# Kernel tuning notes

Hardware: AMD Instinct MI355X
Metric: run time of the kernel (lower is better)

Reference implementation:

```python
import jax, jax.numpy as jnp
import numpy as np

LRELU_SLOPE = 0.2
SQRT2 = 1.4142135623730951

def make_coord(h, w):
    # LIIF make_coord: cell-center coords in [-1, 1]; index 0 is the row (dim -2) coord.
    ys = -1.0 + (2.0 * jnp.arange(h, dtype=jnp.float32) + 1.0) / h
    xs = -1.0 + (2.0 * jnp.arange(w, dtype=jnp.float32) + 1.0) / w
    yy, xx = jnp.meshgrid(ys, xs, indexing='ij')
    return jnp.stack([yy, xx], axis=-1).reshape(h * w, 2)  # [Q, 2]

def style_layer(x, style_vec, scale2, shift, mod_w, mod_b, conv_w, act_b):
    # StyleGAN2-style modulated 3x3 conv + instance norm + (scale2, shift) affine + fused leaky relu.
    s = style_vec @ mod_w.T + mod_b                                   # [B, Cin] modulation
    w = conv_w[None] * s[:, None, :, None, None]                      # [B, Cout, Cin, 3, 3]
    demod = jax.lax.rsqrt(jnp.sum(w * w, axis=(2, 3, 4)) + 1e-8)      # [B, Cout]
    y = jax.lax.conv_general_dilated(x * s[:, :, None, None], conv_w, (1, 1), 'SAME',
                                     dimension_numbers=('NCHW', 'OIHW', 'NCHW'))
    y = y * demod[:, :, None, None]
    mu = jnp.mean(y, axis=(2, 3), keepdims=True)
    var = jnp.var(y, axis=(2, 3), keepdims=True)
    y = (y - mu) * jax.lax.rsqrt(var + 1e-5)                          # InstanceNorm2d (no affine)
    y = y * scale2 + shift
    return jax.nn.leaky_relu(y + act_b[None, :, None, None], LRELU_SLOPE) * SQRT2

def reference(x, scale1, scale2, shift, mod_w, mod_b, conv_w, act_b, w1, b1, w2, b2, out_h, out_w):
    B, C, Hf, Wf = x.shape
    feat = style_layer(x, scale1, scale2, shift, mod_w, mod_b, conv_w, act_b)
    Q = out_h * out_w
    coord = jnp.broadcast_to(make_coord(out_h, out_w)[None], (B, Q, 2))  # [B, Q, 2]
    rx = 1.0 / Hf  # = 2/Hf/2
    ry = 1.0 / Wf
    eps_shift = 1e-6
    feat_flat = feat.reshape(B, C, Hf * Wf).transpose(0, 2, 1)  # [B, Hf*Wf, C]
    preds, areas = [], []
    for vx in (-1, 1):
        for vy in (-1, 1):
            cy = jnp.clip(coord[..., 0] + vx * rx + eps_shift, -1.0 + 1e-6, 1.0 - 1e-6)
            cx = jnp.clip(coord[..., 1] + vy * ry + eps_shift, -1.0 + 1e-6, 1.0 - 1e-6)
            # nearest grid_sample (align_corners=False): idx = floor((c+1)/2 * size)
            iy = jnp.clip(jnp.floor((cy + 1.0) * 0.5 * Hf), 0, Hf - 1).astype(jnp.int32)
            ix = jnp.clip(jnp.floor((cx + 1.0) * 0.5 * Wf), 0, Wf - 1).astype(jnp.int32)
            lin = iy * Wf + ix                                        # [B, Q]
            q_feat = jnp.take_along_axis(feat_flat, lin[..., None], axis=1)  # [B, Q, C]
            qy = -1.0 + (2.0 * iy.astype(jnp.float32) + 1.0) / Hf     # nearest feat-cell coord
            qx = -1.0 + (2.0 * ix.astype(jnp.float32) + 1.0) / Wf
            rel_y = (coord[..., 0] - qy) * Hf
            rel_x = (coord[..., 1] - qx) * Wf
            inp = jnp.concatenate([q_feat, rel_y[..., None], rel_x[..., None]], axis=-1)  # [B,Q,C+2]
            pred = (inp @ w1 + b1) @ w2 + b2                          # two stacked Linears, no act
            preds.append(pred)
            areas.append(jnp.abs(rel_y * rel_x) + 1e-9)
    tot_area = areas[0] + areas[1] + areas[2] + areas[3]
    areas = [areas[3], areas[2], areas[1], areas[0]]  # diagonal swap (local ensemble)
    ret = jnp.zeros_like(preds[0])
    for pred, area in zip(preds, areas):
        ret = ret + pred * (area / tot_area)[..., None]
    return ret  # [B, Q, dim]

def setup_inputs() -> dict:
    key = jax.random.key(0)
    ks = jax.random.split(key, 12)
    B, C, Hf, Wf, S = 4, 64, 64, 64, 512
    return {
        'x': jax.random.normal(ks[0], (B, C, Hf, Wf), jnp.float32),
        'scale1': jax.random.normal(ks[1], (B, S), jnp.float32),
        'scale2': jax.random.normal(ks[2], (B, C, 1, 1), jnp.float32),
        'shift': jax.random.normal(ks[3], (B, C, 1, 1), jnp.float32),
        'mod_w': jax.random.normal(ks[4], (C, S), jnp.float32) * 0.02,
        'mod_b': jnp.ones((C,), jnp.float32),
        'conv_w': jax.random.normal(ks[5], (C, C, 3, 3), jnp.float32) * 0.05,
        'act_b': jax.random.normal(ks[6], (C,), jnp.float32) * 0.02,
        'w1': jax.random.normal(ks[7], (C + 2, 256), jnp.float32) * 0.05,
        'b1': jax.random.normal(ks[8], (256,), jnp.float32) * 0.01,
        'w2': jax.random.normal(ks[9], (256, C), jnp.float32) * 0.05,
        'b2': jax.random.normal(ks[10], (C,), jnp.float32) * 0.01,
        'out_h': 256,
        'out_w': 256,
    }
```

## Files before the change

### kernel.cpp

```cpp
#include <hip/hip_runtime.h>

#define SQRT2F 1.41421356237309515f

typedef __attribute__((ext_vector_type(8))) short bf16x8;
typedef __attribute__((ext_vector_type(4))) float f32x4;

enum : int {
  DM_OFF   = 0,
  BC_OFF   = 256,
  WC_OFF   = 1024,
  P_OFF    = 8192,
  Y_OFF    = 65536,
  WS_FLOATS = Y_OFF + 1048576
};

__device__ __align__(16) float WS[WS_FLOATS];
__device__ __align__(256) unsigned bar_cnt[64];
__device__ __align__(256) unsigned bar_gen[64];

__device__ __forceinline__ unsigned ld_llcu(const unsigned* p) {
  unsigned v;
  asm volatile("global_load_dword %0, %1, off sc0 sc1\n\ts_waitcnt vmcnt(0)"
               : "=v"(v) : "v"(p) : "memory");
  return v;
}
__device__ __forceinline__ float ld_llcf(const float* p) {
  float v;
  asm volatile("global_load_dword %0, %1, off sc0 sc1\n\ts_waitcnt vmcnt(0)"
               : "=v"(v) : "v"(p) : "memory");
  return v;
}
__device__ __forceinline__ void ld_llc4_nw(const float* p, f32x4& v) {
  asm volatile("global_load_dwordx4 %0, %1, off sc0 sc1"
               : "=v"(v) : "v"(p) : "memory");
}
__device__ __forceinline__ void llc_wait() {
  asm volatile("s_waitcnt vmcnt(0)" ::: "memory");
}
__device__ __forceinline__ void stg_llc1(float* p, float v) {
  asm volatile("global_store_dword %0, %1, off sc0 sc1"
               :: "v"(p), "v"(v) : "memory");
}
__device__ __forceinline__ void stg_llc4(float* p, f32x4 v) {
  asm volatile("global_store_dwordx4 %0, %1, off sc0 sc1"
               :: "v"(p), "v"(v) : "memory");
}

struct ConvSh {
  unsigned short Xl[3 * 66 * 64];
  unsigned short Wl[64 * 24 * 8];
  float part[512];
  float s_sh[64];
};
struct GoutSh {
  unsigned short ftb[128][72];
  unsigned short WcTb[64][72];
  float G[100][68];
  float red[2048];
  float A[64], B[64], bcl[64];
};
union ShU { ConvSh c; GoutSh g; };

__device__ __forceinline__ unsigned short f2bf(float v) {
  unsigned int u = __float_as_uint(v);
  u += 0x7fffu + ((u >> 16) & 1u);
  return (unsigned short)(u >> 16);
}

__global__ __launch_bounds__(512) void mega_kernel(
    const float* __restrict__ x,      const float* __restrict__ scale1,
    const float* __restrict__ scale2, const float* __restrict__ shiftp,
    const float* __restrict__ mod_w,  const float* __restrict__ mod_b,
    const float* __restrict__ conv_w, const float* __restrict__ act_b,
    const float* __restrict__ b1,     const float* __restrict__ w2,
    const float* __restrict__ b2,     const float* __restrict__ w1,
    float* __restrict__ out) {
  const int bid = blockIdx.x;
  const int b = bid >> 6;
  const int r = bid & 63;
  const int t = threadIdx.x;
  const int w = t >> 6, lane = t & 63;
  const int l15 = lane & 15, l4 = lane >> 4;

  __shared__ __align__(16) ShU sh;

  {
    const int i = t >> 3, qq = t & 7;
    const float* sv = scale1 + b * 512 + qq * 64;
    const float* mw = mod_w + i * 512 + qq * 64;
    float p = 0.f;
    for (int k = 0; k < 64; ++k) p = fmaf(sv[k], mw[k], p);
    sh.c.part[t] = p;
  }
  __syncthreads();
  if ((t & 7) == 0) {
    const int i = t >> 3;
    float s = mod_b[i];
    #pragma unroll
    for (int k = 0; k < 8; ++k) s += sh.c.part[t + k];
    sh.c.s_sh[i] = s;
  }
  __syncthreads();

  if (r == 0) {
    const int o = t >> 3, qq = t & 7;
    const float* cw = conv_w + o * 576 + qq * 72;
    float d = 0.f;
    #pragma unroll
    for (int ii = 0; ii < 8; ++ii) {
      const float ss = sh.c.s_sh[qq * 8 + ii];
      float wsq = 0.f;
      #pragma unroll
      for (int k = 0; k < 9; ++k) { const float wv = cw[ii * 9 + k]; wsq += wv * wv; }
      d += ss * ss * wsq;
    }
    sh.c.part[t] = d;
    __syncthreads();
    if ((t & 7) == 0) {
      float dd = 1e-8f;
      #pragma unroll
      for (int k = 0; k < 8; ++k) dd += sh.c.part[t + k];
      stg_llc1(&WS[DM_OFF + b * 64 + (t >> 3)], rsqrtf(dd));
    }
    __syncthreads();
  }

  {
    int4* Xz = (int4*)sh.c.Xl;
    int4 z; z.x = z.y = z.z = z.w = 0;
    for (int idx = t; idx < 1584; idx += 512) Xz[idx] = z;
  }
  __syncthreads();

  {
    const int col = t & 63;
    const int tq = t >> 6;
    unsigned int* Xw = (unsigned int*)sh.c.Xl;
    #pragma unroll
    for (int it = 0; it < 12; ++it) {
      const int task = it * 8 + tq;
      const int row3 = task >> 5;
      const int ich = (task & 31) * 2;
      const int rr = r - 1 + row3;
      if (rr >= 0 && rr < 64) {
        const float* xb = x + ((size_t)(b * 64 + ich) << 12) + (rr << 6) + col;
        const float v0 = xb[0] * sh.c.s_sh[ich];
        const float v1 = xb[4096] * sh.c.s_sh[ich + 1];
        const unsigned int u = (unsigned int)f2bf(v0) | ((unsigned int)f2bf(v1) << 16);
        const int colp = col + 1;
        const int byte = ((row3 * 66 + colp) << 7) + ((((ich >> 3)) ^ (colp & 7)) << 4) + ((ich & 7) << 1);
        Xw[byte >> 2] = u;
      }
    }
  }

  const int oh = w >> 2, pg = w & 3;
  f32x4 acc[2];
  acc[0] = (f32x4){0.f, 0.f, 0.f, 0.f};
  acc[1] = (f32x4){0.f, 0.f, 0.f, 0.f};

  const bf16x8* Xv = (const bf16x8*)sh.c.Xl;
  const bf16x8* Wv = (const bf16x8*)sh.c.Wl;
  int4* Wst = (int4*)sh.c.Wl;

  for (int dy = 0; dy < 3; ++dy) {
    __syncthreads();
    #pragma unroll
    for (int i = 0; i < 3; ++i) {
      const int idx = i * 512 + t;
      const int o = idx / 24;
      const int g = idx - o * 24;
      const int dx = g >> 3, gg = g & 7;
      const float* cw = conv_w + o * 576 + (gg * 8) * 9 + dy * 3 + dx;
      int4 v;
      v.x = (int)((unsigned int)f2bf(cw[0])  | ((unsigned int)f2bf(cw[9])  << 16));
      v.y = (int)((unsigned int)f2bf(cw[18]) | ((unsigned int)f2bf(cw[27]) << 16));
      v.z = (int)((unsigned int)f2bf(cw[36]) | ((unsigned int)f2bf(cw[45]) << 16));
      v.w = (int)((unsigned int)f2bf(cw[54]) | ((unsigned int)f2bf(cw[63]) << 16));
      Wst[o * 24 + dx * 8 + (gg ^ (o & 7))] = v;
    }
    __syncthreads();

    #pragma unroll
    for (int dx = 0; dx < 3; ++dx) {
      #pragma unroll
      for (int kh = 0; kh < 2; ++kh) {
        const int kg = kh * 4 + l4;
        bf16x8 afr[2];
        #pragma unroll
        for (int m = 0; m < 2; ++m) {
          const int o = oh * 32 + m * 16 + l15;
          afr[m] = Wv[o * 24 + dx * 8 + (kg ^ (o & 7))];
        }
        const int colp = pg * 16 + l15 + dx;
        const bf16x8 bfr = Xv[((dy * 66 + colp) << 3) + (kg ^ (colp & 7))];
        #pragma unroll
        for (int m = 0; m < 2; ++m)
          acc[m] = __builtin_amdgcn_mfma_f32_16x16x32_bf16(
              afr[m], bfr, acc[m], 0, 0, 0);
      }
    }
  }

  {
    const int px = pg * 16 + l15;
    float* yq = WS + Y_OFF + (((size_t)b * 4096 + r * 64 + px) << 6);
    #pragma unroll
    for (int m = 0; m < 2; ++m)
      stg_llc4(yq + oh * 32 + m * 16 + l4 * 4, acc[m]);
  }

  __syncthreads();
  {
    float* sred = sh.c.part;
    #pragma unroll
    for (int m = 0; m < 2; ++m) {
      #pragma unroll
      for (int j = 0; j < 4; ++j) {
        float s1 = acc[m][j];
        float s2 = acc[m][j] * acc[m][j];
        #pragma unroll
        for (int off = 1; off < 16; off <<= 1) {
          s1 += __shfl_xor(s1, off);
          s2 += __shfl_xor(s2, off);
        }
        if (l15 == 0) {
          const int ol = m * 16 + l4 * 4 + j;
          sred[(w * 32 + ol) * 2 + 0] = s1;
          sred[(w * 32 + ol) * 2 + 1] = s2;
        }
      }
    }
    __syncthreads();
    if (t < 128) {
      const int o = t >> 1, wh = t & 1;
      const int ohh = o >> 5, ol = o & 31;
      float s = 0.f;
      #pragma unroll
      for (int pq = 0; pq < 4; ++pq)
        s += sred[(((ohh * 4 + pq) * 32) + ol) * 2 + wh];
      stg_llc1(&WS[P_OFF + (((size_t)b * 64 + r) * 64 + o) * 2 + wh], s);
    }
  }

  if (t < 17) {
    const int idx = t * 256 + bid;
    if (idx < 4224) {
      const int c = idx >> 6, o = idx & 63;
      const float* r1 = w1 + c * 256;
      float a = 0.f;
      for (int k = 0; k < 256; ++k) a = fmaf(r1[k], w2[k * 64 + o], a);
      stg_llc1(&WS[WC_OFF + idx], a);
    } else if (idx < 4288) {
      const int o = idx - 4224;
      float a = 0.f;
      for (int k = 0; k < 256; ++k) a = fmaf(b1[k], w2[k * 64 + o], a);
      stg_llc1(&WS[BC_OFF + o], a + b2[o]);
    }
  }

  asm volatile("s_waitcnt vmcnt(0)" ::: "memory");
  __syncthreads();
  if (t == 0) {
    unsigned* cnt = &bar_cnt[0];
    unsigned* gen = &bar_gen[0];
    const unsigned g0 = ld_llcu(gen);
    const unsigned old = __hip_atomic_fetch_add(cnt, 1u, __ATOMIC_RELAXED,
                                                __HIP_MEMORY_SCOPE_AGENT);
    if (old == 255u) {
      __hip_atomic_store(cnt, 0u, __ATOMIC_RELAXED, __HIP_MEMORY_SCOPE_AGENT);
      __hip_atomic_fetch_add(gen, 1u, __ATOMIC_RELAXED,
                             __HIP_MEMORY_SCOPE_AGENT);
    } else {
      while (ld_llcu(gen) == g0) __builtin_amdgcn_s_sleep(8);
    }
  }
  __syncthreads();

  const int ty = (bid >> 3) & 7;
  const int tx = bid & 7;
  const int cy_base = ty * 8 - 1, cx_base = tx * 8 - 1;
  float* WcL = &sh.g.G[0][0];

  f32x4 pv0, pv1, pv2, pv3, wv0, wv1, wv2, yv[4];
  int ycell[4], ycq[4];
  bool yok[4];
  {
    const float* Pb = WS + P_OFF + (size_t)b * 8192;
    ld_llc4_nw(Pb + (size_t)t * 4, pv0);
    ld_llc4_nw(Pb + (size_t)(t + 512) * 4, pv1);
    ld_llc4_nw(Pb + (size_t)(t + 1024) * 4, pv2);
    ld_llc4_nw(Pb + (size_t)(t + 1536) * 4, pv3);
    ld_llc4_nw(WS + WC_OFF + (size_t)t * 4, wv0);
    ld_llc4_nw(WS + WC_OFF + (size_t)(t + 512) * 4, wv1);
    const int i4 = 1024 + t;
    const float* wp2 = (i4 < 1056) ? (WS + WC_OFF + (size_t)i4 * 4)
                     : (i4 < 1072) ? (WS + BC_OFF + (size_t)(i4 - 1056) * 4)
                                   : (WS + WC_OFF);
    ld_llc4_nw(wp2, wv2);
    const float* yb = WS + Y_OFF + ((size_t)b << 18);
    #pragma unroll
    for (int k = 0; k < 4; ++k) {
      const int f = t + k * 512;
      const int cell = f >> 4, cq = f & 15;
      const int li = cell / 10, lj = cell - li * 10;
      const int ciy = cy_base + li, cix = cx_base + lj;
      const bool ok = (f < 1600) && ciy >= 0 && ciy < 64 && cix >= 0 && cix < 64;
      ycell[k] = cell; ycq[k] = cq; yok[k] = ok;
      const float* ya = ok ? (yb + (((size_t)(ciy << 6) + cix) << 6) + cq * 4) : yb;
      ld_llc4_nw(ya, yv[k]);
    }
    llc_wait();
  }

  {
    const f32x4 ps = pv0 + pv1 + pv2 + pv3;
    *(f32x4*)&sh.g.red[(t >> 5) * 128 + (t & 31) * 4] = ps;
    *(f32x4*)&WcL[t * 4] = wv0;
    *(f32x4*)&WcL[(t + 512) * 4] = wv1;
    if (1024 + t < 1072) *(f32x4*)&WcL[(1024 + t) * 4] = wv2;
  }
  __syncthreads();

  const int sub = t & 3, chb = sub * 16;
  float4 wa[4], wb[4];
  #pragma unroll
  for (int k = 0; k < 4; ++k) {
    wa[k] = *(const float4*)&WcL[64 * 64 + chb + k * 4];
    wb[k] = *(const float4*)&WcL[65 * 64 + chb + k * 4];
  }
  if (t < 64) {
    float S1 = 0.f, S2 = 0.f;
    #pragma unroll
    for (int m = 0; m < 16; ++m) {
      S1 += sh.g.red[m * 128 + t * 2];
      S2 += sh.g.red[m * 128 + t * 2 + 1];
    }
    const float mu = S1 * (1.f / 4096.f);
    const float var = S2 * (1.f / 4096.f) - mu * mu;
    const float dm = ld_llcf(WS + DM_OFF + b * 64 + t);
    const float rstd = rsqrtf(dm * dm * var + 1e-5f);
    const float A = dm * rstd * scale2[b * 64 + t];
    sh.g.A[t] = A;
    sh.g.B[t] = -mu * A + shiftp[b * 64 + t] + act_b[t];
    sh.g.bcl[t] = WcL[4224 + t];
  }
  {
    const int o = t >> 3, g = t & 7;
    int4 pk;
    unsigned int e0, e1, e2, e3;
    e0 = (unsigned int)f2bf(WcL[(g * 8 + 0) * 64 + o]) |
         ((unsigned int)f2bf(WcL[(g * 8 + 1) * 64 + o]) << 16);
    e1 = (unsigned int)f2bf(WcL[(g * 8 + 2) * 64 + o]) |
         ((unsigned int)f2bf(WcL[(g * 8 + 3) * 64 + o]) << 16);
    e2 = (unsigned int)f2bf(WcL[(g * 8 + 4) * 64 + o]) |
         ((unsigned int)f2bf(WcL[(g * 8 + 5) * 64 + o]) << 16);
    e3 = (unsigned int)f2bf(WcL[(g * 8 + 6) * 64 + o]) |
         ((unsigned int)f2bf(WcL[(g * 8 + 7) * 64 + o]) << 16);
    pk.x = (int)e0; pk.y = (int)e1; pk.z = (int)e2; pk.w = (int)e3;
    *(int4*)&sh.g.WcTb[o][g * 8] = pk;
  }
  __syncthreads();

  {
    const float4* A4 = (const float4*)sh.g.A;
    const float4* B4 = (const float4*)sh.g.B;
    #pragma unroll
    for (int k = 0; k < 4; ++k) {
      if (yok[k]) {
        const float4 Av = A4[ycq[k]], Bv = B4[ycq[k]];
        float f0, f1, f2, f3, u;
        u = yv[k][0] * Av.x + Bv.x; f0 = (u > 0.f ? u : 0.2f * u) * SQRT2F;
        u = yv[k][1] * Av.y + Bv.y; f1 = (u > 0.f ? u : 0.2f * u) * SQRT2F;
        u = yv[k][2] * Av.z + Bv.z; f2 = (u > 0.f ? u : 0.2f * u) * SQRT2F;
        u = yv[k][3] * Av.w + Bv.w; f3 = (u > 0.f ? u : 0.2f * u) * SQRT2F;
        uint2 u2;
        u2.x = (unsigned int)f2bf(f0) | ((unsigned int)f2bf(f1) << 16);
        u2.y = (unsigned int)f2bf(f2) | ((unsigned int)f2bf(f3) << 16);
        *(uint2*)&sh.g.ftb[ycell[k]][ycq[k] * 4] = u2;
      }
    }
  }
  __syncthreads();

  if (w < 7) {
    bf16x8 afr[2];
    #pragma unroll
    for (int kt = 0; kt < 2; ++kt)
      afr[kt] = *(const bf16x8*)&sh.g.ftb[w * 16 + l15][kt * 32 + l4 * 8];
    #pragma unroll
    for (int n = 0; n < 4; ++n) {
      const float bcv = sh.g.bcl[n * 16 + l15];
      f32x4 gacc = (f32x4){bcv, bcv, bcv, bcv};
      #pragma unroll
      for (int kt = 0; kt < 2; ++kt) {
        const bf16x8 bfr =
            *(const bf16x8*)&sh.g.WcTb[n * 16 + l15][kt * 32 + l4 * 8];
        gacc = __builtin_amdgcn_mfma_f32_16x16x32_bf16(afr[kt], bfr, gacc, 0, 0, 0);
      }
      #pragma unroll
      for (int j = 0; j < 4; ++j) {
        const int row = w * 16 + l4 * 4 + j;
        if (row < 100) sh.g.G[row][n * 16 + l15] = gacc[j];
      }
    }
  }
  __syncthreads();

  const float lo = -1.f + 1e-6f, hi = 1.f - 1e-6f;
  #pragma unroll 1
  for (int pass = 0; pass < 8; ++pass) {
    const int qi = pass * 128 + (t >> 2);
    const int oy = (ty << 5) + (qi >> 5), ox = (tx << 5) + (qi & 31);

    const float cy0 = -1.f + (2.f * oy + 1.f) * (1.f / 256.f);
    const float cx0 = -1.f + (2.f * ox + 1.f) * (1.f / 256.f);

    int lcell[4];
    float area[4], rely[4], relx[4];
    int j = 0;
    #pragma unroll
    for (int vx = -1; vx <= 1; vx += 2) {
      #pragma unroll
      for (int vy = -1; vy <= 1; vy += 2) {
        float cy = cy0 + (float)vx * (1.f / 64.f) + 1e-6f;
        cy = fminf(fmaxf(cy, lo), hi);
        float cx = cx0 + (float)vy * (1.f / 64.f) + 1e-6f;
        cx = fminf(fmaxf(cx, lo), hi);
        const float fy = floorf((cy + 1.f) * 32.f);
        const float fx = floorf((cx + 1.f) * 32.f);
        const int iy = (int)fminf(fmaxf(fy, 0.f), 63.f);
        const int ix = (int)fminf(fmaxf(fx, 0.f), 63.f);
        const float qy = -1.f + (2.f * iy + 1.f) * (1.f / 64.f);
        const float qx = -1.f + (2.f * ix + 1.f) * (1.f / 64.f);
        const float ry_ = (cy0 - qy) * 64.f;
        const float rx_ = (cx0 - qx) * 64.f;
        lcell[j] = (iy - cy_base) * 10 + (ix - cx_base);
        rely[j] = ry_; relx[j] = rx_;
        area[j] = fabsf(ry_ * rx_) + 1e-9f;
        ++j;
      }
    }
    const float tot = area[0] + area[1] + area[2] + area[3];
    float wgt[4];
    #pragma unroll
    for (int k = 0; k < 4; ++k) wgt[k] = area[3 - k] / tot;
    const float swy = wgt[0] * rely[0] + wgt[1] * rely[1] + wgt[2] * rely[2] + wgt[3] * rely[3];
    const float swx = wgt[0] * relx[0] + wgt[1] * relx[1] + wgt[2] * relx[2] + wgt[3] * relx[3];

    float4 rr[4];
    #pragma unroll
    for (int k = 0; k < 4; ++k) {
      rr[k].x = swy * wa[k].x + swx * wb[k].x;
      rr[k].y = swy * wa[k].y + swx * wb[k].y;
      rr[k].z = swy * wa[k].z + swx * wb[k].z;
      rr[k].w = swy * wa[k].w + swx * wb[k].w;
    }
    #pragma unroll
    for (int jj = 0; jj < 4; ++jj) {
      const float4* gp = (const float4*)&sh.g.G[lcell[jj]][chb];
      const float wv = wgt[jj];
      #pragma unroll
      for (int k = 0; k < 4; ++k) {
        const float4 gv = gp[k];
        rr[k].x += wv * gv.x; rr[k].y += wv * gv.y;
        rr[k].z += wv * gv.z; rr[k].w += wv * gv.w;
      }
    }
    const size_t gq = ((size_t)b << 16) + (oy << 8) + ox;
    float4* op = (float4*)(out + (gq << 6) + chb);
    #pragma unroll
    for (int k = 0; k < 4; ++k) op[k] = rr[k];
  }
}

extern "C" void kernel_launch(void* const* d_in, const int* in_sizes, int n_in,
                              void* d_out, int out_size, void* d_ws, size_t ws_size,
                              hipStream_t stream) {
  (void)in_sizes; (void)n_in; (void)out_size; (void)d_ws; (void)ws_size;
  const float* x      = (const float*)d_in[0];
  const float* scale1 = (const float*)d_in[1];
  const float* scale2 = (const float*)d_in[2];
  const float* shiftp = (const float*)d_in[3];
  const float* mod_w  = (const float*)d_in[4];
  const float* mod_b  = (const float*)d_in[5];
  const float* conv_w = (const float*)d_in[6];
  const float* act_b  = (const float*)d_in[7];
  const float* w1     = (const float*)d_in[8];
  const float* b1     = (const float*)d_in[9];
  const float* w2     = (const float*)d_in[10];
  const float* b2     = (const float*)d_in[11];
  float* out = (float*)d_out;

  hipLaunchKernelGGL(mega_kernel, dim3(256), dim3(512), 0, stream,
                     x, scale1, scale2, shiftp, mod_w, mod_b, conv_w, act_b,
                     b1, w2, b2, w1, out);
}
```

Before: 68.19 us.

## Precompute bf16 conv weights once globally and use per-batch grid barriers

Every block used to convert the 3x3 conv weights to swizzled bf16 from strided fp32 loads in each dy iteration. Now all blocks convert a slice of the weights once into a global workspace before a new grid-wide barrier, and each block loads the packed tiles with vector loads. The w1·w2 folding moves off the critical tail onto blocks with r=1..9 in each batch. The post-conv barrier becomes a per-batch barrier over 64 blocks. The cost is an extra full-grid barrier early in the kernel and redundant per-batch computation of the folded MLP weights.

```diff
diff --git a/kernel.cpp b/kernel.cpp
--- a/kernel.cpp
+++ b/kernel.cpp
@@ -10,13 +10,16 @@
   BC_OFF   = 256,
   WC_OFF   = 1024,
   P_OFF    = 8192,
+  WB_OFF   = 45056,
   Y_OFF    = 65536,
   WS_FLOATS = Y_OFF + 1048576
 };
 
 __device__ __align__(16) float WS[WS_FLOATS];
-__device__ __align__(256) unsigned bar_cnt[64];
-__device__ __align__(256) unsigned bar_gen[64];
+__device__ __align__(256) unsigned bar_cnt[4 * 64];
+__device__ __align__(256) unsigned bar_gen[4 * 64];
+__device__ __align__(256) unsigned bar2_cnt[64];
+__device__ __align__(256) unsigned bar2_gen[64];
 
 __device__ __forceinline__ unsigned ld_llcu(const unsigned* p) {
   unsigned v;
@@ -102,6 +105,41 @@
   }
   __syncthreads();
 
+  if (t < 18) {
+    const int slot = bid * 18 + t;
+    const int dy = slot / 1536;
+    const int s1 = slot - dy * 1536;
+    const int o = s1 / 24;
+    const int g = s1 - o * 24;
+    const int dx = g >> 3, h = g & 7;
+    const int gg = h ^ (o & 7);
+    const float* cw = conv_w + o * 576 + (gg * 8) * 9 + dy * 3 + dx;
+    f32x4 v;
+    const unsigned e0 = (unsigned)f2bf(cw[0])  | ((unsigned)f2bf(cw[9])  << 16);
+    const unsigned e1 = (unsigned)f2bf(cw[18]) | ((unsigned)f2bf(cw[27]) << 16);
+    const unsigned e2 = (unsigned)f2bf(cw[36]) | ((unsigned)f2bf(cw[45]) << 16);
+    const unsigned e3 = (unsigned)f2bf(cw[54]) | ((unsigned)f2bf(cw[63]) << 16);
+    v[0] = __uint_as_float(e0); v[1] = __uint_as_float(e1);
+    v[2] = __uint_as_float(e2); v[3] = __uint_as_float(e3);
+    stg_llc4(WS + WB_OFF + (size_t)slot * 4, v);
+  }
+  asm volatile("s_waitcnt vmcnt(0)" ::: "memory");
+  __syncthreads();
+  if (t == 0) {
+    const unsigned g0 = ld_llcu(&bar2_gen[0]);
+    const unsigned old = __hip_atomic_fetch_add(&bar2_cnt[0], 1u,
+                          __ATOMIC_RELAXED, __HIP_MEMORY_SCOPE_AGENT);
+    if (old == 255u) {
+      __hip_atomic_store(&bar2_cnt[0], 0u, __ATOMIC_RELAXED,
+                         __HIP_MEMORY_SCOPE_AGENT);
+      __hip_atomic_fetch_add(&bar2_gen[0], 1u, __ATOMIC_RELAXED,
+                             __HIP_MEMORY_SCOPE_AGENT);
+    } else {
+      while (ld_llcu(&bar2_gen[0]) == g0) __builtin_amdgcn_s_sleep(8);
+    }
+  }
+  __syncthreads();
+
   if (r == 0) {
     const int o = t >> 3, qq = t & 7;
     const float* cw = conv_w + o * 576 + qq * 72;
@@ -123,6 +161,29 @@
       stg_llc1(&WS[DM_OFF + b * 64 + (t >> 3)], rsqrtf(dd));
     }
     __syncthreads();
+  }
+
+  if (r >= 1 && r <= 8) {
+    const int idx = (r - 1) * 512 + t;
+    const int c = idx >> 6, o = idx & 63;
+    const float* r1 = w1 + c * 256;
+    float a = 0.f;
+    for (int k = 0; k < 256; ++k) a = fmaf(r1[k], w2[k * 64 + o], a);
+    stg_llc1(&WS[WC_OFF + idx], a);
+  } else if (r == 9) {
+    if (t < 128) {
+      const int idx = 4096 + t;
+      const int c = idx >> 6, o = idx & 63;
+      const float* r1 = w1 + c * 256;
+      float a = 0.f;
+      for (int k = 0; k < 256; ++k) a = fmaf(r1[k], w2[k * 64 + o], a);
+      stg_llc1(&WS[WC_OFF + idx], a);
+    } else if (t < 192) {
+      const int o = t - 128;
+      float a = 0.f;
+      for (int k = 0; k < 256; ++k) a = fmaf(b1[k], w2[k * 64 + o], a);
+      stg_llc1(&WS[BC_OFF + o], a + b2[o]);
+    }
   }
 
   {
@@ -161,23 +222,20 @@
 
   const bf16x8* Xv = (const bf16x8*)sh.c.Xl;
   const bf16x8* Wv = (const bf16x8*)sh.c.Wl;
-  int4* Wst = (int4*)sh.c.Wl;
+  float* Wf = (float*)sh.c.Wl;
 
   for (int dy = 0; dy < 3; ++dy) {
     __syncthreads();
-    #pragma unroll
-    for (int i = 0; i < 3; ++i) {
-      const int idx = i * 512 + t;
-      const int o = idx / 24;
-      const int g = idx - o * 24;
-      const int dx = g >> 3, gg = g & 7;
-      const float* cw = conv_w + o * 576 + (gg * 8) * 9 + dy * 3 + dx;
-      int4 v;
-      v.x = (int)((unsigned int)f2bf(cw[0])  | ((unsigned int)f2bf(cw[9])  << 16));
-      v.y = (int)((unsigned int)f2bf(cw[18]) | ((unsigned int)f2bf(cw[27]) << 16));
-      v.z = (int)((unsigned int)f2bf(cw[36]) | ((unsigned int)f2bf(cw[45]) << 16));
-      v.w = (int)((unsigned int)f2bf(cw[54]) | ((unsigned int)f2bf(cw[63]) << 16));
-      Wst[o * 24 + dx * 8 + (gg ^ (o & 7))] = v;
+    {
+      f32x4 w0, w1v, w2v;
+      const float* src = WS + WB_OFF + (size_t)dy * 6144;
+      ld_llc4_nw(src + (size_t)t * 4, w0);
+      ld_llc4_nw(src + (size_t)(t + 512) * 4, w1v);
+      ld_llc4_nw(src + (size_t)(t + 1024) * 4, w2v);
+      llc_wait();
+      *(f32x4*)&Wf[(size_t)t * 4] = w0;
+      *(f32x4*)&Wf[(size_t)(t + 512) * 4] = w1v;
+      *(f32x4*)&Wf[(size_t)(t + 1024) * 4] = w2v;
     }
     __syncthreads();
 
@@ -243,31 +301,15 @@
     }
   }
 
-  if (t < 17) {
-    const int idx = t * 256 + bid;
-    if (idx < 4224) {
-      const int c = idx >> 6, o = idx & 63;
-      const float* r1 = w1 + c * 256;
-      float a = 0.f;
-      for (int k = 0; k < 256; ++k) a = fmaf(r1[k], w2[k * 64 + o], a);
-      stg_llc1(&WS[WC_OFF + idx], a);
-    } else if (idx < 4288) {
-      const int o = idx - 4224;
-      float a = 0.f;
-      for (int k = 0; k < 256; ++k) a = fmaf(b1[k], w2[k * 64 + o], a);
-      stg_llc1(&WS[BC_OFF + o], a + b2[o]);
-    }
-  }
-
   asm volatile("s_waitcnt vmcnt(0)" ::: "memory");
   __syncthreads();
   if (t == 0) {
-    unsigned* cnt = &bar_cnt[0];
-    unsigned* gen = &bar_gen[0];
+    unsigned* cnt = &bar_cnt[b * 64];
+    unsigned* gen = &bar_gen[b * 64];
     const unsigned g0 = ld_llcu(gen);
     const unsigned old = __hip_atomic_fetch_add(cnt, 1u, __ATOMIC_RELAXED,
                                                 __HIP_MEMORY_SCOPE_AGENT);
-    if (old == 255u) {
+    if (old == 63u) {
       __hip_atomic_store(cnt, 0u, __ATOMIC_RELAXED, __HIP_MEMORY_SCOPE_AGENT);
       __hip_atomic_fetch_add(gen, 1u, __ATOMIC_RELAXED,
                              __HIP_MEMORY_SCOPE_AGENT);
```

Measured after the change: 60.84 us. -10.8%, faster.
